# Performance work log

Hardware: AMD Instinct MI355X
Metric: run time of the kernel (lower is better)

The kernel has to match this reference:

```python
import jax, jax.numpy as jnp
import numpy as np

H = 4096; NH = 32; HD = 128; SCALE = HD ** -0.5
PREFILLS = [1024, 512, 768, 256]; DOFF = sum(PREFILLS)
DEC = 32; LMAX = 512; T = DOFF + DEC
NLORA = 4; RANK = 16
SEG = [0, 648, 1296, 1944, 2592]  # static lora segment offsets (cumsum of lens)
NEG = -1e30


def _rope_tables(pos):
    # pos: int array [...]; returns cos/sin of shape [..., HD]
    inv = 1.0 / (10000.0 ** (jnp.arange(0, HD, 2, dtype=jnp.float32) / HD))
    freqs = pos.astype(jnp.float32)[..., None] * inv
    emb = jnp.concatenate([freqs, freqs], axis=-1)
    return jnp.cos(emb), jnp.sin(emb)


def _apply_rope(x, cos, sin):
    # x: [..., HD]; cos/sin broadcastable to x
    x1, x2 = x[..., :HD // 2], x[..., HD // 2:]
    return x * cos + jnp.concatenate([-x2, x1], axis=-1) * sin


def _add_lora(y, x, wa, wb):
    # Punica add_lora: per-segment y += (x @ wa[i]) @ wb[i], segments static
    for i in range(NLORA):
        s, e = SEG[i], SEG[i + 1]
        y = y.at[s:e].add((x[s:e] @ wa[i]) @ wb[i])
    return y


def setup_inputs() -> dict:
    key = jax.random.key(0)
    ks = jax.random.split(key, 16)
    sc = np.float32(1.0 / np.sqrt(H))
    lsc = np.float32(1.0 / np.sqrt(H))
    inp = {
        "hidden_states": jax.random.normal(ks[0], (T, H), jnp.float32),
        "wq": jax.random.normal(ks[1], (H, H), jnp.float32) * sc,
        "wk": jax.random.normal(ks[2], (H, H), jnp.float32) * sc,
        "wv": jax.random.normal(ks[3], (H, H), jnp.float32) * sc,
        "wo": jax.random.normal(ks[4], (H, H), jnp.float32) * sc,
        "la_q": jax.random.normal(ks[5], (NLORA, H, RANK), jnp.float32) * lsc,
        "lb_q": jax.random.normal(ks[6], (NLORA, RANK, H), jnp.float32) * lsc,
        "la_k": jax.random.normal(ks[7], (NLORA, H, RANK), jnp.float32) * lsc,
        "lb_k": jax.random.normal(ks[8], (NLORA, RANK, H), jnp.float32) * lsc,
        "la_v": jax.random.normal(ks[9], (NLORA, H, RANK), jnp.float32) * lsc,
        "lb_v": jax.random.normal(ks[10], (NLORA, RANK, H), jnp.float32) * lsc,
        "la_o": jax.random.normal(ks[11], (NLORA, H, RANK), jnp.float32) * lsc,
        "lb_o": jax.random.normal(ks[12], (NLORA, RANK, H), jnp.float32) * lsc,
        "k_cache": jax.random.normal(ks[13], (DEC, LMAX, NH, HD), jnp.float32),
        "v_cache": jax.random.normal(ks[14], (DEC, LMAX, NH, HD), jnp.float32),
        "kv_lens": jax.random.randint(ks[15], (DEC,), 0, 450, jnp.int32),
    }
    return inp


def reference(hidden_states, wq, wk, wv, wo, la_q, lb_q, la_k, lb_k,
              la_v, lb_v, la_o, lb_o, k_cache, v_cache, kv_lens):
    # fused QKV + segmented batched LoRA
    q = _add_lora(hidden_states @ wq, hidden_states, la_q, lb_q)
    k = _add_lora(hidden_states @ wk, hidden_states, la_k, lb_k)
    v = _add_lora(hidden_states @ wv, hidden_states, la_v, lb_v)

    outs = []
    # ragged prefill: per-request causal attention with inline rotary (beg=0)
    off = 0
    for s_len in PREFILLS:
        qi = q[off:off + s_len].reshape(s_len, NH, HD)
        ki = k[off:off + s_len].reshape(s_len, NH, HD)
        vi = v[off:off + s_len].reshape(s_len, NH, HD)
        cos, sin = _rope_tables(jnp.arange(s_len))
        cos, sin = cos[:, None, :], sin[:, None, :]
        qi = _apply_rope(qi, cos, sin)
        ki = _apply_rope(ki, cos, sin)
        scores = jnp.einsum('qhd,khd->hqk', qi, ki) * SCALE
        causal = jnp.tril(jnp.ones((s_len, s_len), bool))
        scores = jnp.where(causal[None], scores, NEG)
        p = jax.nn.softmax(scores, axis=-1)
        outs.append(jnp.einsum('hqk,khd->qhd', p, vi).reshape(s_len, H))
        off += s_len

    # paged/batched decode: append new k/v at kv_lens, rope-on-the-fly attention
    qd = q[DOFF:].reshape(DEC, NH, HD)
    kd = k[DOFF:].reshape(DEC, NH, HD)
    vd = v[DOFF:].reshape(DEC, NH, HD)
    b = jnp.arange(DEC)
    kc = k_cache.at[b, kv_lens].set(kd)
    vc = v_cache.at[b, kv_lens].set(vd)
    cosq, sinq = _rope_tables(kv_lens)            # new token position = kv_len
    qd = _apply_rope(qd, cosq[:, None, :], sinq[:, None, :])
    cosk, sink = _rope_tables(jnp.arange(LMAX))   # cache positions 0..LMAX-1
    kc_r = _apply_rope(kc, cosk[None, :, None, :], sink[None, :, None, :])
    scores = jnp.einsum('bhd,blhd->bhl', qd, kc_r) * SCALE
    valid = jnp.arange(LMAX)[None, :] <= kv_lens[:, None]  # [DEC, LMAX]
    scores = jnp.where(valid[:, None, :], scores, NEG)
    p = jax.nn.softmax(scores, axis=-1)
    outs.append(jnp.einsum('bhl,blhd->bhd', p, vc).reshape(DEC, H))

    attn = jnp.concatenate(outs, axis=0)          # [T, H]
    o = attn @ wo
    o = _add_lora(o, attn, la_o, lb_o)
    return o
```

## Files before the change

### kernel.cpp

```cpp
#include <hip/hip_runtime.h>
#include <hip/hip_bf16.h>


#define H_    4096
#define NH_   32
#define HD_   128
#define T_    2592
#define DOFF_ 2560
#define DEC_  32
#define LMAX_ 512
#define RANK_ 16
#define MPAD_ 2816

__constant__ float SCALE_ = 0.08838834764831845f;

typedef __bf16 bf16x8 __attribute__((ext_vector_type(8)));
typedef __bf16 bf16x4 __attribute__((ext_vector_type(4)));
typedef float  f32x4  __attribute__((ext_vector_type(4)));

__device__ __forceinline__ void async_cp16(const __bf16* g, __bf16* l) {
    __builtin_amdgcn_global_load_lds(
        (const __attribute__((address_space(1))) void*)g,
        (__attribute__((address_space(3))) void*)l, 16, 0, 0);
}

__global__ __launch_bounds__(256)
void prep1_kernel(const float* __restrict__ X, __bf16* __restrict__ Xb,
                  const float* __restrict__ la0, const float* __restrict__ la1,
                  const float* __restrict__ la2, __bf16* __restrict__ TMP16,
                  const float* __restrict__ wq, const float* __restrict__ wk,
                  const float* __restrict__ wv, const float* __restrict__ wo,
                  __bf16* __restrict__ wT, __bf16* __restrict__ woT,
                  const float* __restrict__ lbq, const float* __restrict__ lbk,
                  const float* __restrict__ lbv, const float* __restrict__ lbo,
                  __bf16* __restrict__ WB16, __bf16* __restrict__ WBo16,
                  float* __restrict__ cost, float* __restrict__ sint)
{
    const int bid = blockIdx.x;
    const int tid = threadIdx.x;

    if (bid < T_) {
        const int r = bid;
        const float* xr = X + (size_t)r * H_;
        __bf16* br = Xb + (size_t)r * H_;
        #pragma unroll
        for (int i = 0; i < 4; ++i) {
            float4 v = ((const float4*)xr)[tid + i * 256];
            bf16x4 w; w[0] = (__bf16)v.x; w[1] = (__bf16)v.y; w[2] = (__bf16)v.z; w[3] = (__bf16)v.w;
            ((bf16x4*)br)[tid + i * 256] = w;
        }
        const int si = (r < 648) ? 0 : (r < 1296 ? 1 : (r < 1944 ? 2 : 3));
        const int c    = tid & 15;
        const int part = tid >> 4;
        const float* wa0 = la0 + (size_t)si * H_ * RANK_;
        const float* wa1 = la1 + (size_t)si * H_ * RANK_;
        const float* wa2 = la2 + (size_t)si * H_ * RANK_;
        float s0 = 0.f, s1 = 0.f, s2 = 0.f;
        const int h0 = part * 256;
        for (int h = h0; h < h0 + 256; ++h) {
            const float xv = xr[h];
            s0 += xv * wa0[(size_t)h * RANK_ + c];
            s1 += xv * wa1[(size_t)h * RANK_ + c];
            s2 += xv * wa2[(size_t)h * RANK_ + c];
        }
        __shared__ float red[3][16][17];
        red[0][part][c] = s0; red[1][part][c] = s1; red[2][part][c] = s2;
        __syncthreads();
        if (tid < 192) {
            const int z = tid >> 6, cc = tid & 63;
            float t = 0.f;
            if ((cc >> 4) == si) {
                #pragma unroll
                for (int p = 0; p < 16; ++p) t += red[z][p][cc & 15];
            }
            TMP16[((size_t)z * MPAD_ + r) * 64 + cc] = (__bf16)t;
        }
    } else if (bid < T_ + 16384) {
        const int t = bid - T_;
        const int z = t >> 12;
        const int rem = t & 4095;
        const int bx = (rem >> 6) * 64;
        const int by = (rem & 63) * 64;
        const float* W = (z == 0) ? wq : (z == 1 ? wk : (z == 2 ? wv : wo));
        __bf16* To = (z < 3) ? wT + (size_t)z * H_ * H_ : woT;
        __shared__ float s[64][65];
        #pragma unroll
        for (int i = 0; i < 4; ++i) {
            const int idx = i * 256 + tid;
            const int r  = idx >> 4;
            const int c4 = (idx & 15) * 4;
            float4 v = *(const float4*)&W[(size_t)(by + r) * H_ + bx + c4];
            s[r][c4] = v.x; s[r][c4 + 1] = v.y; s[r][c4 + 2] = v.z; s[r][c4 + 3] = v.w;
        }
        __syncthreads();
        #pragma unroll
        for (int i = 0; i < 2; ++i) {
            const int idx = i * 256 + tid;
            const int n  = idx >> 3;
            const int kc = (idx & 7) * 8;
            bf16x8 w;
            #pragma unroll
            for (int j = 0; j < 8; ++j) w[j] = (__bf16)s[kc + j][n];
            *(bf16x8*)&To[(size_t)(bx + n) * H_ + by + kc] = w;
        }
    } else if (bid < T_ + 16384 + 64) {
        const int t = bid - (T_ + 16384);
        const int z = t >> 4;
        const int n = (t & 15) * 256 + tid;
        const float* lb = (z == 0) ? lbq : (z == 1 ? lbk : (z == 2 ? lbv : lbo));
        __bf16* dst = (z < 3) ? WB16 + ((size_t)z * H_ + n) * 64 : WBo16 + (size_t)n * 64;
        __bf16 row[64];
        #pragma unroll
        for (int si = 0; si < 4; ++si)
            #pragma unroll
            for (int c = 0; c < 16; ++c)
                row[si * 16 + c] = (__bf16)lb[((size_t)si * 16 + c) * H_ + n];
        #pragma unroll
        for (int i = 0; i < 8; ++i) *(bf16x8*)&dst[i * 8] = *(const bf16x8*)&row[i * 8];
    } else {
        const int t = bid - (T_ + 16384 + 64);
        const int p = t * 4 + (tid >> 6);
        const int i = tid & 63;
        const float inv = powf(10000.f, -(float)(2 * i) / (float)HD_);
        const float a = (float)p * inv;
        cost[p * 64 + i] = cosf(a);
        sint[p * 64 + i] = sinf(a);
    }
}

__global__ __launch_bounds__(512, 2)
void gemm_qkv(const __bf16* __restrict__ A, const __bf16* __restrict__ Bt,
              const __bf16* __restrict__ TMP16, const __bf16* __restrict__ WB16,
              __bf16* __restrict__ O0, __bf16* __restrict__ O1, __bf16* __restrict__ O2, int M)
{
    const int hw = blockIdx.y * 21 + blockIdx.x;
    const int work = (hw & 7) * 126 + (hw >> 3);
    const int bm0 = (work % 21) * 128;
    const int bn0 = (work / 21) * 256;

    __shared__ __align__(16) __bf16 Asl[3][128 * 64];
    __shared__ __align__(16) __bf16 Bsl[3][256 * 64];

    const int tid = threadIdx.x, lane = tid & 63, wid = tid >> 6;
    const int wr = wid >> 2, wc = wid & 3;
    const int fr = lane & 15, fq = lane >> 4;

    int arow[2], aoff[2], brow[4], boff[4];
    #pragma unroll
    for (int i = 0; i < 2; ++i) {
        const int ci = i * 512 + tid;
        arow[i] = ci >> 3;
        aoff[i] = ((ci & 7) ^ (arow[i] & 7)) * 8;
    }
    #pragma unroll
    for (int i = 0; i < 4; ++i) {
        const int ci = i * 512 + tid;
        brow[i] = ci >> 3;
        boff[i] = ((ci & 7) ^ (brow[i] & 7)) * 8;
    }
    const __bf16* Ab = A  + (size_t)bm0 * H_;
    const __bf16* Bb = Bt + (size_t)bn0 * H_;

    auto stageA = [&](int buf, int kt2) {
        const int kb = kt2 * 64;
        #pragma unroll
        for (int i = 0; i < 2; ++i)
            async_cp16(Ab + (size_t)arow[i] * H_ + kb + aoff[i],
                       &Asl[buf][(i * 512 + wid * 64) * 8]);
    };
    auto stageB1 = [&](int buf, int kt2) {
        async_cp16(Bb + (size_t)brow[0] * H_ + kt2 * 64 + boff[0],
                   &Bsl[buf][(wid * 64) * 8]);
    };
    auto stageB3 = [&](int buf, int kt2) {
        const int kb = kt2 * 64;
        #pragma unroll
        for (int i = 1; i < 4; ++i)
            async_cp16(Bb + (size_t)brow[i] * H_ + kb + boff[i],
                       &Bsl[buf][(i * 512 + wid * 64) * 8]);
    };
    auto rdA = [&](int buf, int kh, int mi) -> bf16x8 {
        const int row = wr * 64 + mi * 16 + fr;
        const int pc  = (kh * 4 + fq) ^ (row & 7);
        return *(const bf16x8*)&Asl[buf][row * 64 + pc * 8];
    };
    auto rdB = [&](int buf, int kh, int nj) -> bf16x8 {
        const int row = wc * 64 + nj * 16 + fr;
        const int pc  = (kh * 4 + fq) ^ (row & 7);
        return *(const bf16x8*)&Bsl[buf][row * 64 + pc * 8];
    };

    f32x4 acc[4][4] = {};

    stageA(0, 0); stageB1(0, 0); stageB3(0, 0);
    stageA(1, 1); stageB1(1, 1); stageB3(1, 1);
    asm volatile("s_waitcnt vmcnt(6)");
    __builtin_amdgcn_sched_barrier(0);
    __builtin_amdgcn_s_barrier();

    const int NT = H_ / 64;
    int cur = 0, nxt = 2;
    for (int kt = 0; kt < NT; ++kt) {
        const bool pf = (kt + 2 < NT);
        bf16x8 af[4], bfr[4];

        #pragma unroll
        for (int mi = 0; mi < 4; ++mi) af[mi] = rdA(cur, 0, mi);
        #pragma unroll
        for (int nj = 0; nj < 4; ++nj) bfr[nj] = rdB(cur, 0, nj);
        if (pf) { stageA(nxt, kt + 2); stageB1(nxt, kt + 2); }
        __builtin_amdgcn_s_barrier();
        asm volatile("s_waitcnt lgkmcnt(0)");
        __builtin_amdgcn_sched_barrier(0);
        __builtin_amdgcn_s_setprio(1);
        #pragma unroll
        for (int mi = 0; mi < 4; ++mi)
            #pragma unroll
            for (int nj = 0; nj < 4; ++nj)
                acc[mi][nj] = __builtin_amdgcn_mfma_f32_16x16x32_bf16(af[mi], bfr[nj], acc[mi][nj], 0, 0, 0);
        __builtin_amdgcn_s_setprio(0);
        __builtin_amdgcn_s_barrier();

        #pragma unroll
        for (int mi = 0; mi < 4; ++mi) af[mi] = rdA(cur, 1, mi);
        #pragma unroll
        for (int nj = 0; nj < 4; ++nj) bfr[nj] = rdB(cur, 1, nj);
        if (pf) stageB3(nxt, kt + 2);
        __builtin_amdgcn_s_barrier();
        asm volatile("s_waitcnt lgkmcnt(0)");
        __builtin_amdgcn_sched_barrier(0);
        __builtin_amdgcn_s_setprio(1);
        #pragma unroll
        for (int mi = 0; mi < 4; ++mi)
            #pragma unroll
            for (int nj = 0; nj < 4; ++nj)
                acc[mi][nj] = __builtin_amdgcn_mfma_f32_16x16x32_bf16(af[mi], bfr[nj], acc[mi][nj], 0, 0, 0);
        __builtin_amdgcn_s_setprio(0);
        if (pf)               asm volatile("s_waitcnt vmcnt(6)");
        else if (kt + 1 < NT) asm volatile("s_waitcnt vmcnt(0)");
        __builtin_amdgcn_sched_barrier(0);
        __builtin_amdgcn_s_barrier();

        cur = (cur == 2) ? 0 : cur + 1;
        nxt = (nxt == 2) ? 0 : nxt + 1;
    }

    const int colbase = bn0 + wc * 64;
    const int mat = colbase >> 12;
    __bf16* O = (mat == 0) ? O0 : (mat == 1 ? O1 : O2);
    const __bf16* TPm = TMP16 + (size_t)mat * MPAD_ * 64;
    bf16x8 aT[4][2], bW[4][2];
    #pragma unroll
    for (int mi = 0; mi < 4; ++mi)
        #pragma unroll
        for (int kh = 0; kh < 2; ++kh)
            aT[mi][kh] = *(const bf16x8*)&TPm[(size_t)(bm0 + wr * 64 + mi * 16 + fr) * 64 + kh * 32 + fq * 8];
    #pragma unroll
    for (int nj = 0; nj < 4; ++nj)
        #pragma unroll
        for (int kh = 0; kh < 2; ++kh)
            bW[nj][kh] = *(const bf16x8*)&WB16[(size_t)(colbase + nj * 16 + fr) * 64 + kh * 32 + fq * 8];
    #pragma unroll
    for (int mi = 0; mi < 4; ++mi)
        #pragma unroll
        for (int nj = 0; nj < 4; ++nj) {
            acc[mi][nj] = __builtin_amdgcn_mfma_f32_16x16x32_bf16(aT[mi][0], bW[nj][0], acc[mi][nj], 0, 0, 0);
            acc[mi][nj] = __builtin_amdgcn_mfma_f32_16x16x32_bf16(aT[mi][1], bW[nj][1], acc[mi][nj], 0, 0, 0);
        }
    #pragma unroll
    for (int mi = 0; mi < 4; ++mi)
        #pragma unroll
        for (int nj = 0; nj < 4; ++nj) {
            const int cc = (colbase + nj * 16 + fr) & 4095;
            #pragma unroll
            for (int rr = 0; rr < 4; ++rr) {
                const int row = bm0 + wr * 64 + mi * 16 + fq * 4 + rr;
                if (row < M) O[(size_t)row * H_ + cc] = (__bf16)acc[mi][nj][rr];
            }
        }
}

__global__ __launch_bounds__(512, 2)
void gemm_out(const __bf16* __restrict__ A, const __bf16* __restrict__ Bt,
              const __bf16* __restrict__ TMPo16, const __bf16* __restrict__ WBo16,
              float* __restrict__ C, int M, int Ntot)
{
    const int NY = gridDim.y;
    const int total = gridDim.x * NY;
    const int bid = blockIdx.x * NY + blockIdx.y;
    const int q = total >> 3, r8 = total & 7;
    const int xcd = bid & 7, j = bid >> 3;
    const int swz = (xcd < r8 ? xcd * (q + 1) : r8 * (q + 1) + (xcd - r8) * q) + j;
    const int bm0 = (swz / NY) * 256;
    const int bn0 = (swz % NY) * 192;

    __shared__ __align__(16) __bf16 Asl[2][256 * 64];
    __shared__ __align__(16) __bf16 Bsl[2][192 * 64];

    const int tid = threadIdx.x, lane = tid & 63, wid = tid >> 6;
    const int wr = wid >> 2, wc = wid & 3;
    const int fr = lane & 15, fq = lane >> 4;

    int arow[4], aoff[4], brow[3], boff[3];
    #pragma unroll
    for (int i = 0; i < 4; ++i) {
        const int ci = i * 512 + tid;
        arow[i] = ci >> 3;
        aoff[i] = ((ci & 7) ^ (arow[i] & 7)) * 8;
    }
    #pragma unroll
    for (int i = 0; i < 3; ++i) {
        const int ci = i * 512 + tid;
        brow[i] = ci >> 3;
        boff[i] = ((ci & 7) ^ (brow[i] & 7)) * 8;
    }
    const __bf16* Ab = A  + (size_t)bm0 * H_;
    const __bf16* Bb = Bt + (size_t)bn0 * H_;

    auto stage = [&](int buf, int kt1) {
        const int kb = kt1 * 64;
        #pragma unroll
        for (int i = 0; i < 4; ++i)
            async_cp16(Ab + (size_t)arow[i] * H_ + kb + aoff[i],
                       &Asl[buf][(i * 512 + wid * 64) * 8]);
        #pragma unroll
        for (int i = 0; i < 3; ++i)
            async_cp16(Bb + (size_t)brow[i] * H_ + kb + boff[i],
                       &Bsl[buf][(i * 512 + wid * 64) * 8]);
    };
    auto rdA = [&](int buf, int kh, int mi) -> bf16x8 {
        const int row = wr * 128 + mi * 16 + fr;
        const int kc  = kh * 4 + fq;
        return *(const bf16x8*)&Asl[buf][row * 64 + ((kc ^ (row & 7)) << 3)];
    };
    auto rdB = [&](int buf, int kh, int nj) -> bf16x8 {
        const int row = wc * 48 + nj * 16 + fr;
        const int kc  = kh * 4 + fq;
        return *(const bf16x8*)&Bsl[buf][row * 64 + ((kc ^ (row & 7)) << 3)];
    };

    f32x4 acc[8][3] = {};

    stage(0, 0);
    asm volatile("s_waitcnt vmcnt(0)");
    __builtin_amdgcn_sched_barrier(0);
    __builtin_amdgcn_s_barrier();

    const int NT = H_ / 64;
    for (int kt = 0; kt < NT; ++kt) {
        const int cur = kt & 1, nb = cur ^ 1;
        const bool pf = (kt + 1 < NT);
        bf16x8 af[8], bfr[3];

        #pragma unroll
        for (int mi = 0; mi < 8; ++mi) af[mi] = rdA(cur, 0, mi);
        #pragma unroll
        for (int nj = 0; nj < 3; ++nj) bfr[nj] = rdB(cur, 0, nj);
        if (pf) stage(nb, kt + 1);
        __builtin_amdgcn_s_barrier();
        asm volatile("s_waitcnt lgkmcnt(0)");
        __builtin_amdgcn_sched_barrier(0);
        __builtin_amdgcn_s_setprio(1);
        #pragma unroll
        for (int mi = 0; mi < 8; ++mi)
            #pragma unroll
            for (int nj = 0; nj < 3; ++nj)
                acc[mi][nj] = __builtin_amdgcn_mfma_f32_16x16x32_bf16(af[mi], bfr[nj], acc[mi][nj], 0, 0, 0);
        __builtin_amdgcn_s_setprio(0);
        __builtin_amdgcn_s_barrier();

        #pragma unroll
        for (int mi = 0; mi < 8; ++mi) af[mi] = rdA(cur, 1, mi);
        #pragma unroll
        for (int nj = 0; nj < 3; ++nj) bfr[nj] = rdB(cur, 1, nj);
        __builtin_amdgcn_s_barrier();
        asm volatile("s_waitcnt lgkmcnt(0)");
        __builtin_amdgcn_sched_barrier(0);
        __builtin_amdgcn_s_setprio(1);
        #pragma unroll
        for (int mi = 0; mi < 8; ++mi)
            #pragma unroll
            for (int nj = 0; nj < 3; ++nj)
                acc[mi][nj] = __builtin_amdgcn_mfma_f32_16x16x32_bf16(af[mi], bfr[nj], acc[mi][nj], 0, 0, 0);
        __builtin_amdgcn_s_setprio(0);
        asm volatile("s_waitcnt vmcnt(0)");
        __builtin_amdgcn_sched_barrier(0);
        __builtin_amdgcn_s_barrier();
    }

    const int colw = bn0 + wc * 48;
    bf16x8 aT[8][2], bW[3][2];
    #pragma unroll
    for (int mi = 0; mi < 8; ++mi)
        #pragma unroll
        for (int kh = 0; kh < 2; ++kh)
            aT[mi][kh] = *(const bf16x8*)&TMPo16[(size_t)(bm0 + wr * 128 + mi * 16 + fr) * 64 + kh * 32 + fq * 8];
    #pragma unroll
    for (int nj = 0; nj < 3; ++nj)
        #pragma unroll
        for (int kh = 0; kh < 2; ++kh)
            bW[nj][kh] = *(const bf16x8*)&WBo16[(size_t)(colw + nj * 16 + fr) * 64 + kh * 32 + fq * 8];
    #pragma unroll
    for (int mi = 0; mi < 8; ++mi)
        #pragma unroll
        for (int nj = 0; nj < 3; ++nj) {
            acc[mi][nj] = __builtin_amdgcn_mfma_f32_16x16x32_bf16(aT[mi][0], bW[nj][0], acc[mi][nj], 0, 0, 0);
            acc[mi][nj] = __builtin_amdgcn_mfma_f32_16x16x32_bf16(aT[mi][1], bW[nj][1], acc[mi][nj], 0, 0, 0);
        }
    #pragma unroll
    for (int mi = 0; mi < 8; ++mi)
        #pragma unroll
        for (int nj = 0; nj < 3; ++nj) {
            const int col = colw + nj * 16 + fr;
            if (col < Ntot) {
                #pragma unroll
                for (int rr = 0; rr < 4; ++rr) {
                    const int row = bm0 + wr * 128 + mi * 16 + fq * 4 + rr;
                    if (row < M) C[(size_t)row * H_ + col] = acc[mi][nj][rr];
                }
            }
        }
}

__global__ __launch_bounds__(256)
void lora_tmp_bf16_kernel(const __bf16* __restrict__ X,
                          const float* __restrict__ la, __bf16* __restrict__ TMPo16)
{
    const int r = blockIdx.x;
    const int si = (r < 648) ? 0 : (r < 1296 ? 1 : (r < 1944 ? 2 : 3));
    const float* wa = la + (size_t)si * H_ * RANK_;
    const int c    = threadIdx.x & 15;
    const int part = threadIdx.x >> 4;
    const __bf16* xr = X + (size_t)r * H_;
    float s = 0.f;
    const int h0 = part * 256;
    for (int h = h0; h < h0 + 256; ++h) s += (float)xr[h] * wa[(size_t)h * RANK_ + c];
    __shared__ float red[16][17];
    red[part][c] = s;
    __syncthreads();
    if (threadIdx.x < 64) {
        const int cc = threadIdx.x;
        float t = 0.f;
        if ((cc >> 4) == si) {
            #pragma unroll
            for (int p = 0; p < 16; ++p) t += red[p][cc & 15];
        }
        TMPo16[(size_t)r * 64 + cc] = (__bf16)t;
    }
}

__global__ __launch_bounds__(256)
void post1_kernel(__bf16* __restrict__ q16, __bf16* __restrict__ k16,
                  const __bf16* __restrict__ v16, __bf16* __restrict__ vT,
                  const int* __restrict__ kv_lens,
                  const float* __restrict__ cost, const float* __restrict__ sint)
{
    const int bid = blockIdx.x;
    const int tid = threadIdx.x;

    if (bid < T_) {
        const int r = bid;
        int pos; bool dok;
        if (r < DOFF_) {
            if      (r < 1024) pos = r;
            else if (r < 1536) pos = r - 1024;
            else if (r < 2304) pos = r - 1536;
            else               pos = r - 2304;
            dok = true;
        } else {
            pos = kv_lens[r - DOFF_];
            dok = false;
        }
        const int h = tid >> 3, sub = tid & 7;
        const int i0 = sub * 8;
        const size_t b1 = (size_t)r * H_ + h * HD_ + i0;
        const size_t b2 = b1 + 64;

        float cs[8], sn[8];
        #pragma unroll
        for (int j = 0; j < 8; ++j) { cs[j] = cost[pos * 64 + i0 + j]; sn[j] = sint[pos * 64 + i0 + j]; }

        {
            bf16x8 x1 = *(const bf16x8*)&q16[b1], x2 = *(const bf16x8*)&q16[b2];
            bf16x8 o1, o2;
            #pragma unroll
            for (int j = 0; j < 8; ++j) {
                const float f1 = (float)x1[j], f2 = (float)x2[j];
                o1[j] = (__bf16)(f1 * cs[j] - f2 * sn[j]);
                o2[j] = (__bf16)(f2 * cs[j] + f1 * sn[j]);
            }
            *(bf16x8*)&q16[b1] = o1; *(bf16x8*)&q16[b2] = o2;
        }
        if (dok) {
            bf16x8 x1 = *(const bf16x8*)&k16[b1], x2 = *(const bf16x8*)&k16[b2];
            bf16x8 o1, o2;
            #pragma unroll
            for (int j = 0; j < 8; ++j) {
                const float f1 = (float)x1[j], f2 = (float)x2[j];
                o1[j] = (__bf16)(f1 * cs[j] - f2 * sn[j]);
                o2[j] = (__bf16)(f2 * cs[j] + f1 * sn[j]);
            }
            *(bf16x8*)&k16[b1] = o1; *(bf16x8*)&k16[b2] = o2;
        }
    } else {
        const int t = bid - T_;
        const int tb = t % 40;
        const int h  = t / 40;
        __shared__ __bf16 s[64][136];
        #pragma unroll
        for (int i = 0; i < 4; ++i) {
            const int idx = i * 256 + tid;
            const int row = idx >> 4;
            const int c8  = (idx & 15) * 8;
            *(bf16x8*)&s[row][c8] = *(const bf16x8*)&v16[(size_t)(tb * 64 + row) * H_ + h * HD_ + c8];
        }
        __syncthreads();
        #pragma unroll
        for (int i = 0; i < 4; ++i) {
            const int idx = i * 256 + tid;
            const int d = idx >> 3;
            const int c = idx & 7;
            bf16x8 w;
            #pragma unroll
            for (int j = 0; j < 8; ++j) w[j] = s[c * 8 + j][d];
            *(bf16x8*)&vT[(size_t)(h * HD_ + d) * T_ + tb * 64 + c * 8] = w;
        }
    }
}

__global__ __launch_bounds__(256)
void prefill_attn_wave(const __bf16* __restrict__ q16, const __bf16* __restrict__ k16,
                       const __bf16* __restrict__ vT, __bf16* __restrict__ attn16)
{
    const int tid = threadIdx.x, lane = tid & 63, wid = tid >> 6;
    const int h = blockIdx.x / 40;
    const int g = (blockIdx.x % 40) * 4 + wid;
    int soff, gq;
    if      (g < 64)  { soff = 0;    gq = g; }
    else if (g < 96)  { soff = 1024; gq = g - 64; }
    else if (g < 144) { soff = 1536; gq = g - 96; }
    else              { soff = 2304; gq = g - 144; }
    const int qoff = gq * 16;
    const int fr = lane & 15, fq = lane >> 4;

    __shared__ __align__(16) __bf16 Pl[4][16 * 32];
    __bf16* Plw = Pl[wid];

    const int grow0 = soff + qoff;
    bf16x8 qf[4];
    #pragma unroll
    for (int ks = 0; ks < 4; ++ks)
        qf[ks] = *(const bf16x8*)&q16[(size_t)(grow0 + fr) * H_ + h * HD_ + ks * 32 + fq * 8];

    float m[4], l[4];
    #pragma unroll
    for (int r = 0; r < 4; ++r) { m[r] = -1e30f; l[r] = 0.f; }
    f32x4 o[8] = {};

    const int ntiles = (qoff + 15) / 32 + 1;
    const __bf16* Kb = k16 + h * HD_;
    const __bf16* Vb = vT + (size_t)h * HD_ * T_;

    for (int t = 0; t < ntiles; ++t) {
        const int kt = t * 32;

        f32x4 s[2] = {};
        #pragma unroll
        for (int sub = 0; sub < 2; ++sub)
            #pragma unroll
            for (int ks = 0; ks < 4; ++ks) {
                bf16x8 bk = *(const bf16x8*)&Kb[(size_t)(soff + kt + sub * 16 + fr) * H_ + ks * 32 + fq * 8];
                s[sub] = __builtin_amdgcn_mfma_f32_16x16x32_bf16(qf[ks], bk, s[sub], 0, 0, 0);
            }

        float p[2][4];
        #pragma unroll
        for (int sub = 0; sub < 2; ++sub)
            #pragma unroll
            for (int r = 0; r < 4; ++r) {
                const int qpos = qoff + fq * 4 + r;
                const int kpos = kt + sub * 16 + fr;
                p[sub][r] = (kpos <= qpos) ? s[sub][r] * SCALE_ : -1e30f;
            }
        float tm2[4];
        #pragma unroll
        for (int r = 0; r < 4; ++r) {
            float tm = fmaxf(p[0][r], p[1][r]);
            tm = fmaxf(tm, __shfl_xor(tm, 1));
            tm = fmaxf(tm, __shfl_xor(tm, 2));
            tm = fmaxf(tm, __shfl_xor(tm, 4));
            tm = fmaxf(tm, __shfl_xor(tm, 8));
            tm2[r] = tm;
        }
        bool need = false;
        #pragma unroll
        for (int r = 0; r < 4; ++r) need |= (tm2[r] > m[r] + 8.f);
        if (__any(need)) {
            #pragma unroll
            for (int r = 0; r < 4; ++r) {
                const float mn = fmaxf(m[r], tm2[r]);
                const float f  = __expf(m[r] - mn);
                m[r] = mn;
                l[r] *= f;
                #pragma unroll
                for (int c = 0; c < 8; ++c) o[c][r] *= f;
            }
        }
        #pragma unroll
        for (int r = 0; r < 4; ++r) {
            float ls = 0.f;
            #pragma unroll
            for (int sub = 0; sub < 2; ++sub) {
                p[sub][r] = __expf(p[sub][r] - m[r]);
                ls += p[sub][r];
            }
            l[r] += ls;
        }

        #pragma unroll
        for (int sub = 0; sub < 2; ++sub)
            #pragma unroll
            for (int r = 0; r < 4; ++r) {
                const int qr = fq * 4 + r;
                const int col = sub * 16 + fr;
                Plw[qr * 32 + ((((col >> 3) ^ (qr & 3)) & 3) * 8) + (col & 7)] = (__bf16)p[sub][r];
            }
        bf16x8 pa = *(const bf16x8*)&Plw[fr * 32 + (((fq ^ (fr & 3)) & 3) * 8)];

        #pragma unroll
        for (int c = 0; c < 8; ++c) {
            bf16x8 bv = *(const bf16x8*)&Vb[(size_t)(c * 16 + fr) * T_ + soff + kt + fq * 8];
            o[c] = __builtin_amdgcn_mfma_f32_16x16x32_bf16(pa, bv, o[c], 0, 0, 0);
        }
    }

    float inv[4];
    #pragma unroll
    for (int r = 0; r < 4; ++r) {
        float ls = l[r];
        ls += __shfl_xor(ls, 1); ls += __shfl_xor(ls, 2);
        ls += __shfl_xor(ls, 4); ls += __shfl_xor(ls, 8);
        inv[r] = 1.f / ls;
    }
    #pragma unroll
    for (int c = 0; c < 8; ++c)
        #pragma unroll
        for (int r = 0; r < 4; ++r)
            attn16[(size_t)(grow0 + fq * 4 + r) * H_ + h * HD_ + c * 16 + fr] = (__bf16)(o[c][r] * inv[r]);
}

__global__ __launch_bounds__(256)
void decode_attn_kernel(const __bf16* __restrict__ q16, const __bf16* __restrict__ k16,
                        const __bf16* __restrict__ v16, const float* __restrict__ kc,
                        const float* __restrict__ vc, const int* __restrict__ kv_lens,
                        const float* __restrict__ cost, const float* __restrict__ sint,
                        __bf16* __restrict__ attn16)
{
    const int b = blockIdx.x, h = blockIdx.y;
    const int kvlen = kv_lens[b];
    const int L = kvlen + 1;
    const int tid = threadIdx.x, lane = tid & 63, w = tid >> 6;

    __shared__ float sc_s[LMAX_];
    __shared__ float red[4];
    __shared__ float oacc[HD_];

    const __bf16* qrow = q16 + (size_t)(DOFF_ + b) * H_ + h * HD_;
    const float q1 = (float)qrow[lane], q2 = (float)qrow[lane + 64];
    const __bf16* kdrow = k16 + (size_t)(DOFF_ + b) * H_ + h * HD_;

    for (int l = w; l < L; l += 4) {
        float k1, k2;
        if (l == kvlen) { k1 = (float)kdrow[lane]; k2 = (float)kdrow[lane + 64]; }
        else {
            const float* src = kc + (((size_t)b * LMAX_ + l) * NH_ + h) * HD_;
            k1 = src[lane]; k2 = src[lane + 64];
        }
        const float c = cost[l * 64 + lane], s = sint[l * 64 + lane];
        float d = q1 * (k1 * c - k2 * s) + q2 * (k2 * c + k1 * s);
        #pragma unroll
        for (int off = 1; off < 64; off <<= 1) d += __shfl_xor(d, off);
        if (lane == 0) sc_s[l] = d * SCALE_;
    }
    __syncthreads();

    float mx = -1e30f;
    for (int i = tid; i < L; i += 256) mx = fmaxf(mx, sc_s[i]);
    #pragma unroll
    for (int off = 1; off < 64; off <<= 1) mx = fmaxf(mx, __shfl_xor(mx, off));
    if (lane == 0) red[w] = mx;
    __syncthreads();
    mx = fmaxf(fmaxf(red[0], red[1]), fmaxf(red[2], red[3]));
    __syncthreads();

    float sum = 0.f;
    for (int i = tid; i < L; i += 256) { const float e = __expf(sc_s[i] - mx); sc_s[i] = e; sum += e; }
    #pragma unroll
    for (int off = 1; off < 64; off <<= 1) sum += __shfl_xor(sum, off);
    if (lane == 0) red[w] = sum;
    __syncthreads();
    sum = red[0] + red[1] + red[2] + red[3];
    const float inv = 1.f / sum;

    const int d = tid & 127, team = tid >> 7;
    const __bf16* vdrow = v16 + (size_t)(DOFF_ + b) * H_ + h * HD_;
    float acc = 0.f;
    for (int l = team; l < L; l += 2) {
        float vv;
        if (l == kvlen) vv = (float)vdrow[d];
        else            vv = vc[(((size_t)b * LMAX_ + l) * NH_ + h) * HD_ + d];
        acc += sc_s[l] * vv;
    }
    if (team == 1) oacc[d] = acc;
    __syncthreads();
    if (team == 0) attn16[(size_t)(DOFF_ + b) * H_ + h * HD_ + d] = (__bf16)((acc + oacc[d]) * inv);
}

extern "C" void kernel_launch(void* const* d_in, const int* in_sizes, int n_in,
                              void* d_out, int out_size, void* d_ws, size_t ws_size,
                              hipStream_t stream)
{
    const float* hs     = (const float*)d_in[0];
    const float* wq     = (const float*)d_in[1];
    const float* wk     = (const float*)d_in[2];
    const float* wv     = (const float*)d_in[3];
    const float* wo     = (const float*)d_in[4];
    const float* la_q   = (const float*)d_in[5];
    const float* lb_q   = (const float*)d_in[6];
    const float* la_k   = (const float*)d_in[7];
    const float* lb_k   = (const float*)d_in[8];
    const float* la_v   = (const float*)d_in[9];
    const float* lb_v   = (const float*)d_in[10];
    const float* la_o   = (const float*)d_in[11];
    const float* lb_o   = (const float*)d_in[12];
    const float* kcache = (const float*)d_in[13];
    const float* vcache = (const float*)d_in[14];
    const int*   kvlen  = (const int*)d_in[15];
    float* out = (float*)d_out;

    float*  costab = (float*)d_ws;
    float*  sintab = costab + 1024 * 64;
    __bf16* TMP16  = (__bf16*)(sintab + 1024 * 64);
    __bf16* TMPo16 = TMP16 + (size_t)3 * MPAD_ * 64;
    __bf16* WB16   = TMPo16 + (size_t)MPAD_ * 64;
    __bf16* WBo16  = WB16 + (size_t)3 * H_ * 64;
    __bf16* q16    = WBo16 + (size_t)4352 * 64;
    __bf16* k16    = q16 + (size_t)T_ * H_;
    __bf16* v16    = k16 + (size_t)T_ * H_;
    __bf16* hsb    = v16 + (size_t)T_ * H_;
    __bf16* wT     = hsb + (size_t)MPAD_ * H_;
    __bf16* woT    = wT + (size_t)3 * H_ * H_;
    __bf16* vT     = woT + (size_t)H_ * H_;
    __bf16* attn16 = hsb;

    prep1_kernel<<<dim3(T_ + 16384 + 64 + 256), dim3(256), 0, stream>>>(
        hs, hsb, la_q, la_k, la_v, TMP16,
        wq, wk, wv, wo, wT, woT,
        lb_q, lb_k, lb_v, lb_o, WB16, WBo16, costab, sintab);
    gemm_qkv<<<dim3(21, 48), dim3(512), 0, stream>>>(
        hsb, wT, TMP16, WB16, q16, k16, v16, T_);
    post1_kernel<<<dim3(T_ + 1280), dim3(256), 0, stream>>>(
        q16, k16, v16, vT, kvlen, costab, sintab);
    prefill_attn_wave<<<dim3(1280), dim3(256), 0, stream>>>(q16, k16, vT, attn16);
    decode_attn_kernel<<<dim3(DEC_, NH_), dim3(256), 0, stream>>>(q16, k16, v16, kcache, vcache,
                                                                  kvlen, costab, sintab, attn16);
    lora_tmp_bf16_kernel<<<dim3(T_), dim3(256), 0, stream>>>(attn16, la_o, TMPo16);
    gemm_out<<<dim3(11, 22), dim3(512), 0, stream>>>(
        attn16, woT, TMPo16, WBo16, out, T_, H_);
}
```

Measured before the change: 1.077 ms.

## Split fused prep kernels and reuse the wq slot for the transposed wo

Splits the monolithic prep and post kernels into separate single-purpose launches: rope tables, hidden-state cast with LoRA-A, weight transpose, LoRA-B build, rope, and V transpose. The wo transpose is deferred until after attention and written into the wT buffer, overwriting the wq slot so the workspace shrinks and the woT region is no longer needed. This reduces the memory footprint and may improve cache locality for gemm_out, at the cost of several extra kernel launches and the loss of intra-kernel overlap between heterogeneous work.

```diff
diff --git a/kernel.cpp b/kernel.cpp
--- a/kernel.cpp
+++ b/kernel.cpp
@@ -25,107 +25,125 @@
 }
 
 __global__ __launch_bounds__(256)
-void prep1_kernel(const float* __restrict__ X, __bf16* __restrict__ Xb,
-                  const float* __restrict__ la0, const float* __restrict__ la1,
-                  const float* __restrict__ la2, __bf16* __restrict__ TMP16,
-                  const float* __restrict__ wq, const float* __restrict__ wk,
-                  const float* __restrict__ wv, const float* __restrict__ wo,
-                  __bf16* __restrict__ wT, __bf16* __restrict__ woT,
-                  const float* __restrict__ lbq, const float* __restrict__ lbk,
-                  const float* __restrict__ lbv, const float* __restrict__ lbo,
-                  __bf16* __restrict__ WB16, __bf16* __restrict__ WBo16,
-                  float* __restrict__ cost, float* __restrict__ sint)
-{
-    const int bid = blockIdx.x;
+void hs_prep_kernel(const float* __restrict__ X, __bf16* __restrict__ Xb,
+                    const float* __restrict__ la0, const float* __restrict__ la1,
+                    const float* __restrict__ la2, __bf16* __restrict__ TMP16)
+{
+    const int r = blockIdx.x;
     const int tid = threadIdx.x;
-
-    if (bid < T_) {
-        const int r = bid;
-        const float* xr = X + (size_t)r * H_;
-        __bf16* br = Xb + (size_t)r * H_;
-        #pragma unroll
-        for (int i = 0; i < 4; ++i) {
-            float4 v = ((const float4*)xr)[tid + i * 256];
-            bf16x4 w; w[0] = (__bf16)v.x; w[1] = (__bf16)v.y; w[2] = (__bf16)v.z; w[3] = (__bf16)v.w;
-            ((bf16x4*)br)[tid + i * 256] = w;
-        }
-        const int si = (r < 648) ? 0 : (r < 1296 ? 1 : (r < 1944 ? 2 : 3));
-        const int c    = tid & 15;
-        const int part = tid >> 4;
-        const float* wa0 = la0 + (size_t)si * H_ * RANK_;
-        const float* wa1 = la1 + (size_t)si * H_ * RANK_;
-        const float* wa2 = la2 + (size_t)si * H_ * RANK_;
-        float s0 = 0.f, s1 = 0.f, s2 = 0.f;
-        const int h0 = part * 256;
-        for (int h = h0; h < h0 + 256; ++h) {
-            const float xv = xr[h];
-            s0 += xv * wa0[(size_t)h * RANK_ + c];
-            s1 += xv * wa1[(size_t)h * RANK_ + c];
-            s2 += xv * wa2[(size_t)h * RANK_ + c];
-        }
-        __shared__ float red[3][16][17];
-        red[0][part][c] = s0; red[1][part][c] = s1; red[2][part][c] = s2;
-        __syncthreads();
-        if (tid < 192) {
-            const int z = tid >> 6, cc = tid & 63;
-            float t = 0.f;
-            if ((cc >> 4) == si) {
-                #pragma unroll
-                for (int p = 0; p < 16; ++p) t += red[z][p][cc & 15];
-            }
-            TMP16[((size_t)z * MPAD_ + r) * 64 + cc] = (__bf16)t;
-        }
-    } else if (bid < T_ + 16384) {
-        const int t = bid - T_;
-        const int z = t >> 12;
-        const int rem = t & 4095;
-        const int bx = (rem >> 6) * 64;
-        const int by = (rem & 63) * 64;
-        const float* W = (z == 0) ? wq : (z == 1 ? wk : (z == 2 ? wv : wo));
-        __bf16* To = (z < 3) ? wT + (size_t)z * H_ * H_ : woT;
-        __shared__ float s[64][65];
-        #pragma unroll
-        for (int i = 0; i < 4; ++i) {
-            const int idx = i * 256 + tid;
-            const int r  = idx >> 4;
-            const int c4 = (idx & 15) * 4;
-            float4 v = *(const float4*)&W[(size_t)(by + r) * H_ + bx + c4];
-            s[r][c4] = v.x; s[r][c4 + 1] = v.y; s[r][c4 + 2] = v.z; s[r][c4 + 3] = v.w;
-        }
-        __syncthreads();
-        #pragma unroll
-        for (int i = 0; i < 2; ++i) {
-            const int idx = i * 256 + tid;
-            const int n  = idx >> 3;
-            const int kc = (idx & 7) * 8;
-            bf16x8 w;
-            #pragma unroll
-            for (int j = 0; j < 8; ++j) w[j] = (__bf16)s[kc + j][n];
-            *(bf16x8*)&To[(size_t)(bx + n) * H_ + by + kc] = w;
-        }
-    } else if (bid < T_ + 16384 + 64) {
-        const int t = bid - (T_ + 16384);
-        const int z = t >> 4;
-        const int n = (t & 15) * 256 + tid;
-        const float* lb = (z == 0) ? lbq : (z == 1 ? lbk : (z == 2 ? lbv : lbo));
-        __bf16* dst = (z < 3) ? WB16 + ((size_t)z * H_ + n) * 64 : WBo16 + (size_t)n * 64;
-        __bf16 row[64];
-        #pragma unroll
-        for (int si = 0; si < 4; ++si)
-            #pragma unroll
-            for (int c = 0; c < 16; ++c)
-                row[si * 16 + c] = (__bf16)lb[((size_t)si * 16 + c) * H_ + n];
-        #pragma unroll
-        for (int i = 0; i < 8; ++i) *(bf16x8*)&dst[i * 8] = *(const bf16x8*)&row[i * 8];
-    } else {
-        const int t = bid - (T_ + 16384 + 64);
-        const int p = t * 4 + (tid >> 6);
-        const int i = tid & 63;
-        const float inv = powf(10000.f, -(float)(2 * i) / (float)HD_);
-        const float a = (float)p * inv;
-        cost[p * 64 + i] = cosf(a);
-        sint[p * 64 + i] = sinf(a);
-    }
+    const float* xr = X + (size_t)r * H_;
+    __bf16* br = Xb + (size_t)r * H_;
+    #pragma unroll
+    for (int i = 0; i < 4; ++i) {
+        float4 v = ((const float4*)xr)[tid + i * 256];
+        bf16x4 w; w[0] = (__bf16)v.x; w[1] = (__bf16)v.y; w[2] = (__bf16)v.z; w[3] = (__bf16)v.w;
+        ((bf16x4*)br)[tid + i * 256] = w;
+    }
+
+    const int si = (r < 648) ? 0 : (r < 1296 ? 1 : (r < 1944 ? 2 : 3));
+    const int c    = tid & 15;
+    const int part = tid >> 4;
+    const float* wa0 = la0 + (size_t)si * H_ * RANK_;
+    const float* wa1 = la1 + (size_t)si * H_ * RANK_;
+    const float* wa2 = la2 + (size_t)si * H_ * RANK_;
+    float s0 = 0.f, s1 = 0.f, s2 = 0.f;
+    const int h0 = part * 256;
+    for (int h = h0; h < h0 + 256; ++h) {
+        const float xv = xr[h];
+        s0 += xv * wa0[(size_t)h * RANK_ + c];
+        s1 += xv * wa1[(size_t)h * RANK_ + c];
+        s2 += xv * wa2[(size_t)h * RANK_ + c];
+    }
+    __shared__ float red[3][16][17];
+    red[0][part][c] = s0; red[1][part][c] = s1; red[2][part][c] = s2;
+    __syncthreads();
+    if (tid < 192) {
+        const int z = tid >> 6, cc = tid & 63;
+        float t = 0.f;
+        if ((cc >> 4) == si) {
+            #pragma unroll
+            for (int p = 0; p < 16; ++p) t += red[z][p][cc & 15];
+        }
+        TMP16[((size_t)z * MPAD_ + r) * 64 + cc] = (__bf16)t;
+    }
+}
+
+__global__ __launch_bounds__(256)
+void transpose_bf16_kernel(const float* __restrict__ W0, const float* __restrict__ W1,
+                           const float* __restrict__ W2,
+                           __bf16* __restrict__ T0, __bf16* __restrict__ T1, __bf16* __restrict__ T2)
+{
+    const float* W = (blockIdx.z == 0) ? W0 : (blockIdx.z == 1 ? W1 : W2);
+    __bf16* To     = (blockIdx.z == 0) ? T0 : (blockIdx.z == 1 ? T1 : T2);
+    __shared__ float s[64][65];
+    const int bx = blockIdx.x * 64;
+    const int by = blockIdx.y * 64;
+    const int tid = threadIdx.x;
+    #pragma unroll
+    for (int i = 0; i < 4; ++i) {
+        const int idx = i * 256 + tid;
+        const int r  = idx >> 4;
+        const int c4 = (idx & 15) * 4;
+        float4 v = *(const float4*)&W[(size_t)(by + r) * H_ + bx + c4];
+        s[r][c4] = v.x; s[r][c4 + 1] = v.y; s[r][c4 + 2] = v.z; s[r][c4 + 3] = v.w;
+    }
+    __syncthreads();
+    #pragma unroll
+    for (int i = 0; i < 2; ++i) {
+        const int idx = i * 256 + tid;
+        const int n  = idx >> 3;
+        const int kc = (idx & 7) * 8;
+        bf16x8 w;
+        #pragma unroll
+        for (int j = 0; j < 8; ++j) w[j] = (__bf16)s[kc + j][n];
+        *(bf16x8*)&To[(size_t)(bx + n) * H_ + by + kc] = w;
+    }
+}
+
+__global__ __launch_bounds__(256)
+void lora_tmp_bf16_kernel(const __bf16* __restrict__ X,
+                          const float* __restrict__ la, __bf16* __restrict__ TMPo16)
+{
+    const int r = blockIdx.x;
+    const int si = (r < 648) ? 0 : (r < 1296 ? 1 : (r < 1944 ? 2 : 3));
+    const float* wa = la + (size_t)si * H_ * RANK_;
+    const int c    = threadIdx.x & 15;
+    const int part = threadIdx.x >> 4;
+    const __bf16* xr = X + (size_t)r * H_;
+    float s = 0.f;
+    const int h0 = part * 256;
+    for (int h = h0; h < h0 + 256; ++h) s += (float)xr[h] * wa[(size_t)h * RANK_ + c];
+    __shared__ float red[16][17];
+    red[part][c] = s;
+    __syncthreads();
+    if (threadIdx.x < 64) {
+        const int cc = threadIdx.x;
+        float t = 0.f;
+        if ((cc >> 4) == si) {
+            #pragma unroll
+            for (int p = 0; p < 16; ++p) t += red[p][cc & 15];
+        }
+        TMPo16[(size_t)r * 64 + cc] = (__bf16)t;
+    }
+}
+
+__global__ __launch_bounds__(256)
+void wb_build_kernel(const float* __restrict__ lbq, const float* __restrict__ lbk,
+                     const float* __restrict__ lbv, const float* __restrict__ lbo,
+                     __bf16* __restrict__ WB16, __bf16* __restrict__ WBo16)
+{
+    const int z = blockIdx.x;
+    const int n = blockIdx.y * 256 + threadIdx.x;
+    const float* lb = (z == 0) ? lbq : (z == 1 ? lbk : (z == 2 ? lbv : lbo));
+    __bf16* dst = (z < 3) ? WB16 + ((size_t)z * H_ + n) * 64 : WBo16 + (size_t)n * 64;
+    __bf16 row[64];
+    #pragma unroll
+    for (int si = 0; si < 4; ++si)
+        #pragma unroll
+        for (int c = 0; c < 16; ++c)
+            row[si * 16 + c] = (__bf16)lb[((size_t)si * 16 + c) * H_ + n];
+    #pragma unroll
+    for (int i = 0; i < 8; ++i) *(bf16x8*)&dst[i * 8] = *(const bf16x8*)&row[i * 8];
 }
 
 __global__ __launch_bounds__(512, 2)
@@ -422,109 +440,91 @@
         }
 }
 
+__global__ void rope_table_kernel(float* __restrict__ cost, float* __restrict__ sint)
+{
+    const int p = blockIdx.x;
+    const int i = threadIdx.x;
+    const float inv = powf(10000.f, -(float)(2 * i) / (float)HD_);
+    const float a = (float)p * inv;
+    cost[p * 64 + i] = cosf(a);
+    sint[p * 64 + i] = sinf(a);
+}
+
 __global__ __launch_bounds__(256)
-void lora_tmp_bf16_kernel(const __bf16* __restrict__ X,
-                          const float* __restrict__ la, __bf16* __restrict__ TMPo16)
+void rope16_kernel(__bf16* __restrict__ q16, __bf16* __restrict__ k16,
+                   const int* __restrict__ kv_lens,
+                   const float* __restrict__ cost, const float* __restrict__ sint)
 {
     const int r = blockIdx.x;
-    const int si = (r < 648) ? 0 : (r < 1296 ? 1 : (r < 1944 ? 2 : 3));
-    const float* wa = la + (size_t)si * H_ * RANK_;
-    const int c    = threadIdx.x & 15;
-    const int part = threadIdx.x >> 4;
-    const __bf16* xr = X + (size_t)r * H_;
-    float s = 0.f;
-    const int h0 = part * 256;
-    for (int h = h0; h < h0 + 256; ++h) s += (float)xr[h] * wa[(size_t)h * RANK_ + c];
-    __shared__ float red[16][17];
-    red[part][c] = s;
-    __syncthreads();
-    if (threadIdx.x < 64) {
-        const int cc = threadIdx.x;
-        float t = 0.f;
-        if ((cc >> 4) == si) {
-            #pragma unroll
-            for (int p = 0; p < 16; ++p) t += red[p][cc & 15];
-        }
-        TMPo16[(size_t)r * 64 + cc] = (__bf16)t;
+    int pos; bool dok;
+    if (r < DOFF_) {
+        if      (r < 1024) pos = r;
+        else if (r < 1536) pos = r - 1024;
+        else if (r < 2304) pos = r - 1536;
+        else               pos = r - 2304;
+        dok = true;
+    } else {
+        pos = kv_lens[r - DOFF_];
+        dok = false;
+    }
+    const int tid = threadIdx.x;
+    const int h = tid >> 3, sub = tid & 7;
+    const int i0 = sub * 8;
+    const size_t b1 = (size_t)r * H_ + h * HD_ + i0;
+    const size_t b2 = b1 + 64;
+
+    float cs[8], sn[8];
+    #pragma unroll
+    for (int j = 0; j < 8; ++j) { cs[j] = cost[pos * 64 + i0 + j]; sn[j] = sint[pos * 64 + i0 + j]; }
+
+    {
+        bf16x8 x1 = *(const bf16x8*)&q16[b1], x2 = *(const bf16x8*)&q16[b2];
+        bf16x8 o1, o2;
+        #pragma unroll
+        for (int j = 0; j < 8; ++j) {
+            const float f1 = (float)x1[j], f2 = (float)x2[j];
+            o1[j] = (__bf16)(f1 * cs[j] - f2 * sn[j]);
+            o2[j] = (__bf16)(f2 * cs[j] + f1 * sn[j]);
+        }
+        *(bf16x8*)&q16[b1] = o1; *(bf16x8*)&q16[b2] = o2;
+    }
+    if (dok) {
+        bf16x8 x1 = *(const bf16x8*)&k16[b1], x2 = *(const bf16x8*)&k16[b2];
+        bf16x8 o1, o2;
+        #pragma unroll
+        for (int j = 0; j < 8; ++j) {
+            const float f1 = (float)x1[j], f2 = (float)x2[j];
+            o1[j] = (__bf16)(f1 * cs[j] - f2 * sn[j]);
+            o2[j] = (__bf16)(f2 * cs[j] + f1 * sn[j]);
+        }
+        *(bf16x8*)&k16[b1] = o1; *(bf16x8*)&k16[b2] = o2;
     }
 }
 
 __global__ __launch_bounds__(256)
-void post1_kernel(__bf16* __restrict__ q16, __bf16* __restrict__ k16,
-                  const __bf16* __restrict__ v16, __bf16* __restrict__ vT,
-                  const int* __restrict__ kv_lens,
-                  const float* __restrict__ cost, const float* __restrict__ sint)
-{
-    const int bid = blockIdx.x;
+void transpose_v_kernel(const __bf16* __restrict__ v16, __bf16* __restrict__ vT)
+{
+    __shared__ __bf16 s[64][136];
+    const int tb = blockIdx.x;
+    const int h  = blockIdx.y;
     const int tid = threadIdx.x;
-
-    if (bid < T_) {
-        const int r = bid;
-        int pos; bool dok;
-        if (r < DOFF_) {
-            if      (r < 1024) pos = r;
-            else if (r < 1536) pos = r - 1024;
-            else if (r < 2304) pos = r - 1536;
-            else               pos = r - 2304;
-            dok = true;
-        } else {
-            pos = kv_lens[r - DOFF_];
-            dok = false;
-        }
-        const int h = tid >> 3, sub = tid & 7;
-        const int i0 = sub * 8;
-        const size_t b1 = (size_t)r * H_ + h * HD_ + i0;
-        const size_t b2 = b1 + 64;
-
-        float cs[8], sn[8];
-        #pragma unroll
-        for (int j = 0; j < 8; ++j) { cs[j] = cost[pos * 64 + i0 + j]; sn[j] = sint[pos * 64 + i0 + j]; }
-
-        {
-            bf16x8 x1 = *(const bf16x8*)&q16[b1], x2 = *(const bf16x8*)&q16[b2];
-            bf16x8 o1, o2;
-            #pragma unroll
-            for (int j = 0; j < 8; ++j) {
-                const float f1 = (float)x1[j], f2 = (float)x2[j];
-                o1[j] = (__bf16)(f1 * cs[j] - f2 * sn[j]);
-                o2[j] = (__bf16)(f2 * cs[j] + f1 * sn[j]);
-            }
-            *(bf16x8*)&q16[b1] = o1; *(bf16x8*)&q16[b2] = o2;
-        }
-        if (dok) {
-            bf16x8 x1 = *(const bf16x8*)&k16[b1], x2 = *(const bf16x8*)&k16[b2];
-            bf16x8 o1, o2;
-            #pragma unroll
-            for (int j = 0; j < 8; ++j) {
-                const float f1 = (float)x1[j], f2 = (float)x2[j];
-                o1[j] = (__bf16)(f1 * cs[j] - f2 * sn[j]);
-                o2[j] = (__bf16)(f2 * cs[j] + f1 * sn[j]);
-            }
-            *(bf16x8*)&k16[b1] = o1; *(bf16x8*)&k16[b2] = o2;
-        }
-    } else {
-        const int t = bid - T_;
-        const int tb = t % 40;
-        const int h  = t / 40;
-        __shared__ __bf16 s[64][136];
-        #pragma unroll
-        for (int i = 0; i < 4; ++i) {
-            const int idx = i * 256 + tid;
-            const int row = idx >> 4;
-            const int c8  = (idx & 15) * 8;
-            *(bf16x8*)&s[row][c8] = *(const bf16x8*)&v16[(size_t)(tb * 64 + row) * H_ + h * HD_ + c8];
-        }
-        __syncthreads();
-        #pragma unroll
-        for (int i = 0; i < 4; ++i) {
-            const int idx = i * 256 + tid;
-            const int d = idx >> 3;
-            const int c = idx & 7;
-            bf16x8 w;
-            #pragma unroll
-            for (int j = 0; j < 8; ++j) w[j] = s[c * 8 + j][d];
-            *(bf16x8*)&vT[(size_t)(h * HD_ + d) * T_ + tb * 64 + c * 8] = w;
-        }
+    #pragma unroll
+    for (int i = 0; i < 4; ++i) {
+        const int idx = i * 256 + tid;
+        const int row = idx >> 4;
+        const int c8  = (idx & 15) * 8;
+        *(bf16x8*)&s[row][c8] = *(const bf16x8*)&v16[(size_t)(tb * 64 + row) * H_ + h * HD_ + c8];
+    }
+    __syncthreads();
+    #pragma unroll
+    for (int i = 0; i < 4; ++i) {
+        const int idx = i * 256 + tid;
+        const int d = idx >> 3;
+        const int c = idx & 7;
+        bf16x8 w;
+        #pragma unroll
+        for (int j = 0; j < 8; ++j) w[j] = s[c * 8 + j][d];
+        *(bf16x8*)&vT[(size_t)(h * HD_ + d) * T_ + tb * 64 + c * 8] = w;
     }
 }
 
@@ -749,22 +749,23 @@
     __bf16* v16    = k16 + (size_t)T_ * H_;
     __bf16* hsb    = v16 + (size_t)T_ * H_;
     __bf16* wT     = hsb + (size_t)MPAD_ * H_;
-    __bf16* woT    = wT + (size_t)3 * H_ * H_;
-    __bf16* vT     = woT + (size_t)H_ * H_;
+    __bf16* vT     = wT + (size_t)H_ * H_;
     __bf16* attn16 = hsb;
 
-    prep1_kernel<<<dim3(T_ + 16384 + 64 + 256), dim3(256), 0, stream>>>(
-        hs, hsb, la_q, la_k, la_v, TMP16,
-        wq, wk, wv, wo, wT, woT,
-        lb_q, lb_k, lb_v, lb_o, WB16, WBo16, costab, sintab);
+    rope_table_kernel<<<dim3(1024), dim3(64), 0, stream>>>(costab, sintab);
+    hs_prep_kernel<<<dim3(T_), dim3(256), 0, stream>>>(hs, hsb, la_q, la_k, la_v, TMP16);
+    transpose_bf16_kernel<<<dim3(64, 64, 3), dim3(256), 0, stream>>>(
+        wq, wk, wv, wT, wT + (size_t)H_ * H_, wT + (size_t)2 * H_ * H_);
+    wb_build_kernel<<<dim3(4, 16), dim3(256), 0, stream>>>(lb_q, lb_k, lb_v, lb_o, WB16, WBo16);
     gemm_qkv<<<dim3(21, 48), dim3(512), 0, stream>>>(
         hsb, wT, TMP16, WB16, q16, k16, v16, T_);
-    post1_kernel<<<dim3(T_ + 1280), dim3(256), 0, stream>>>(
-        q16, k16, v16, vT, kvlen, costab, sintab);
+    rope16_kernel<<<dim3(T_), dim3(256), 0, stream>>>(q16, k16, kvlen, costab, sintab);
+    transpose_v_kernel<<<dim3(40, 32), dim3(256), 0, stream>>>(v16, vT);
     prefill_attn_wave<<<dim3(1280), dim3(256), 0, stream>>>(q16, k16, vT, attn16);
     decode_attn_kernel<<<dim3(DEC_, NH_), dim3(256), 0, stream>>>(q16, k16, v16, kcache, vcache,
                                                                   kvlen, costab, sintab, attn16);
+    transpose_bf16_kernel<<<dim3(64, 64, 1), dim3(256), 0, stream>>>(wo, wo, wo, wT, wT, wT);
     lora_tmp_bf16_kernel<<<dim3(T_), dim3(256), 0, stream>>>(attn16, la_o, TMPo16);
     gemm_out<<<dim3(11, 22), dim3(512), 0, stream>>>(
-        attn16, woT, TMPo16, WBo16, out, T_, H_);
-}
+        attn16, wT, TMPo16, WBo16, out, T_, H_);
+}
```

Measured after the change: 1.065 ms. About the same (-1.1%).
